# Performance work log

Hardware: AMD Instinct MI355X
Metric: run time of the kernel (lower is better)

The kernel has to match this reference:

```python
import jax, jax.numpy as jnp
import numpy as np

S, B, D = 2048, 2, 1024          # seq, batch, hidden
E, K = 64, 2                     # num_experts, top_k
I, SI = 512, 512                 # moe_intermediate, shared_expert_intermediate
CAP = 256                        # per-expert capacity; mean load = S*B*K/E = 128, 256 is >16 sigma -> no drops


def setup_inputs() -> dict:
    key = jax.random.key(0)
    ks = jax.random.split(key, 8)
    sc = lambda d: 1.0 / np.sqrt(d)
    return {
        "hidden_states": jax.random.normal(ks[0], (S, B, D), jnp.float32),
        "router_w": jax.random.normal(ks[1], (E, D), jnp.float32) * sc(D),          # FujiTopKRouter.weight
        "gate_up_proj": jax.random.normal(ks[2], (E, 2 * I, D), jnp.float32) * sc(D),
        "down_proj": jax.random.normal(ks[3], (E, D, I), jnp.float32) * sc(I),
        "sh_gate_w": jax.random.normal(ks[4], (SI, D), jnp.float32) * sc(D),
        "sh_up_w": jax.random.normal(ks[5], (SI, D), jnp.float32) * sc(D),
        "sh_down_w": jax.random.normal(ks[6], (D, SI), jnp.float32) * sc(SI),
        "sh_expert_gate_w": jax.random.normal(ks[7], (1, D), jnp.float32) * sc(D),
    }


def _moe(x, router_w, gate_up_proj, down_proj, sh_gate_w, sh_up_w, sh_down_w, sh_expert_gate_w):
    T = x.shape[0]
    # ---- shared expert (SwiGLU) + sigmoid gate ----
    shared = jnp.dot(jax.nn.silu(x @ sh_gate_w.T) * (x @ sh_up_w.T), sh_down_w.T)
    shared = jax.nn.sigmoid(x @ sh_expert_gate_w.T) * shared                      # [T, D]
    # ---- router: softmax (fp32) -> top-k -> normalize ----
    probs = jax.nn.softmax((x @ router_w.T).astype(jnp.float32), axis=-1)         # [T, E]
    top_w, top_i = jax.lax.top_k(probs, K)                                        # [T, K]
    top_w = top_w / (jnp.sum(top_w, axis=-1, keepdims=True) + 1e-9)
    top_w = top_w.astype(x.dtype)
    # ---- dispatch: permute (token, slot) pairs into fixed-capacity expert buffers ----
    e_f = top_i.reshape(-1)                                                       # [T*K] expert id per pair
    w_f = top_w.reshape(-1)                                                       # [T*K]
    tok = jnp.arange(T * K) // K                                                  # [T*K] source token
    oh = jax.nn.one_hot(e_f, E, dtype=jnp.int32)                                  # [T*K, E]
    pos = jnp.sum(jnp.cumsum(oh, axis=0) * oh, axis=-1) - 1                       # slot within expert
    buf = jnp.zeros((E, CAP, D), x.dtype).at[e_f, pos].set(x[tok])                # [E, C, D]
    # ---- per-expert SwiGLU as batched GEMMs ----
    h = jnp.einsum('ecd,eid->eci', buf, gate_up_proj)                             # [E, C, 2I]
    g, u = jnp.split(h, 2, axis=-1)
    y = jnp.einsum('eci,edi->ecd', jax.nn.silu(g) * u, down_proj)                 # [E, C, D]
    # ---- combine: gather back, weight, scatter-add to tokens ----
    routed = jnp.zeros_like(x).at[tok].add(y[e_f, pos] * w_f[:, None])            # [T, D]
    return shared + routed, probs


def reference(hidden_states, router_w, gate_up_proj, down_proj,
              sh_gate_w, sh_up_w, sh_down_w, sh_expert_gate_w):
    s, b, d = hidden_states.shape
    x = hidden_states.reshape(-1, d)
    out, router_logits = _moe(x, router_w, gate_up_proj, down_proj,
                              sh_gate_w, sh_up_w, sh_down_w, sh_expert_gate_w)
    return out.reshape(s, b, d), router_logits
```

## Files before the change

kernel.cpp:

```cpp
#include <hip/hip_runtime.h>
#include <hip/hip_bf16.h>
#include <stdint.h>

#define T_TOK 4096
#define DDIM  1024
#define NEXP  64
#define IDIM  512
#define SIDIM 512
#define CAP   256
#define KZ    8

typedef __attribute__((ext_vector_type(4))) float f32x4;
typedef __attribute__((ext_vector_type(8))) short bf16x8;

#define WAITV4 asm volatile("s_waitcnt vmcnt(4)" ::: "memory")
#define WAITV0 asm volatile("s_waitcnt vmcnt(0)" ::: "memory")
#define WAITL0 asm volatile("s_waitcnt lgkmcnt(0)" ::: "memory")
#define MEMBAR asm volatile("" ::: "memory")

__device__ __forceinline__ bf16x8 cvt8(f32x4 a, f32x4 b) {
    union { __hip_bfloat162 h[4]; bf16x8 v; } u;
    u.h[0] = __float22bfloat162_rn(make_float2(a[0], a[1]));
    u.h[1] = __float22bfloat162_rn(make_float2(a[2], a[3]));
    u.h[2] = __float22bfloat162_rn(make_float2(b[0], b[1]));
    u.h[3] = __float22bfloat162_rn(make_float2(b[2], b[3]));
    return u.v;
}
__device__ __forceinline__ short f2bs(float f) {
    union { __hip_bfloat16 h; short s; } u; u.h = __float2bfloat16(f); return u.s;
}

__device__ __forceinline__ void gload16(const void* g, void* l) {
    __builtin_amdgcn_global_load_lds((const __attribute__((address_space(1))) void*)g,
                                     (__attribute__((address_space(3))) void*)l, 16, 0, 0);
}

__device__ __forceinline__ bf16x8 frag32(const char* reg0, int row, int s) {
    const char* p = reg0 + row * 128;
    int sw = row & 7;
    f32x4 lo = *(const f32x4*)(p + (((2 * s) ^ sw) << 4));
    f32x4 hi = *(const f32x4*)(p + (((2 * s + 1) ^ sw) << 4));
    return cvt8(lo, hi);
}
__device__ __forceinline__ bf16x8 fragbf(const char* reg0, int row, int s) {
    return *(const bf16x8*)(reg0 + row * 64 + (((s) ^ (row & 3)) << 4));
}

__global__ __launch_bounds__(256) void logits_kernel(const float* __restrict__ X,
                                                     const float* __restrict__ RW,
                                                     float* __restrict__ lpart) {
    __shared__ float sX[64 * 33];
    __shared__ float sW[64 * 33];
    int m0 = blockIdx.x * 64;
    int kz = blockIdx.y;
    int kbase = kz * (DDIM / KZ);
    int tid = threadIdx.x;
    int tg = tid >> 4;
    int eg = tid & 15;
    float acc[4][4] = {};
    for (int k0 = 0; k0 < DDIM / KZ; k0 += 32) {
        __syncthreads();
#pragma unroll
        for (int i = 0; i < 8; ++i) {
            int idx = i * 256 + tid;
            int r = idx >> 5, c = idx & 31;
            sX[r * 33 + c] = X[(size_t)(m0 + r) * DDIM + kbase + k0 + c];
            sW[r * 33 + c] = RW[(size_t)r * DDIM + kbase + k0 + c];
        }
        __syncthreads();
#pragma unroll 4
        for (int k = 0; k < 32; ++k) {
            float xv[4], wv[4];
#pragma unroll
            for (int i = 0; i < 4; ++i) xv[i] = sX[(tg * 4 + i) * 33 + k];
#pragma unroll
            for (int j = 0; j < 4; ++j) wv[j] = sW[(eg * 4 + j) * 33 + k];
#pragma unroll
            for (int i = 0; i < 4; ++i)
#pragma unroll
                for (int j = 0; j < 4; ++j) acc[i][j] += xv[i] * wv[j];
        }
    }
    float* outp = lpart + (size_t)kz * T_TOK * NEXP;
#pragma unroll
    for (int i = 0; i < 4; ++i)
#pragma unroll
        for (int j = 0; j < 4; ++j)
            outp[(size_t)(m0 + tg * 4 + i) * NEXP + eg * 4 + j] = acc[i][j];
}

__global__ __launch_bounds__(256) void topk_kernel(const float* __restrict__ lpart,
                                                   const float* __restrict__ X,
                                                   const float* __restrict__ SEG,
                                                   float* __restrict__ probs_out,
                                                   int* __restrict__ counts,
                                                   int* __restrict__ tok_slot,
                                                   float* __restrict__ w_slot,
                                                   float* __restrict__ gate_sh) {
    int lane = threadIdx.x & 63;
    int wv   = threadIdx.x >> 6;
    int t    = blockIdx.x * 4 + wv;
    size_t li = (size_t)t * NEXP + lane;
    float l = 0.f;
#pragma unroll
    for (int z = 0; z < KZ; ++z) l += lpart[(size_t)z * T_TOK * NEXP + li];
    float mx = l;
    for (int s = 32; s; s >>= 1) mx = fmaxf(mx, __shfl_xor(mx, s));
    float e = __expf(l - mx);
    float sum = e;
    for (int s = 32; s; s >>= 1) sum += __shfl_xor(sum, s);
    float prob = e / sum;
    probs_out[li] = prob;
    float v = prob; int idx = lane;
    for (int s = 32; s; s >>= 1) {
        float ov = __shfl_xor(v, s); int oi = __shfl_xor(idx, s);
        if (ov > v || (ov == v && oi < idx)) { v = ov; idx = oi; }
    }
    float v1 = v; int i1 = idx;
    v = (lane == i1) ? -1e30f : prob; idx = lane;
    for (int s = 32; s; s >>= 1) {
        float ov = __shfl_xor(v, s); int oi = __shfl_xor(idx, s);
        if (ov > v || (ov == v && oi < idx)) { v = ov; idx = oi; }
    }
    float v2 = v; int i2 = idx;
    float denom = v1 + v2 + 1e-9f;
    if (lane == 0) {
        int s1 = atomicAdd(&counts[i1], 1);
        if (s1 < CAP) { tok_slot[i1 * CAP + s1] = t; w_slot[i1 * CAP + s1] = v1 / denom; }
        int s2 = atomicAdd(&counts[i2], 1);
        if (s2 < CAP) { tok_slot[i2 * CAP + s2] = t; w_slot[i2 * CAP + s2] = v2 / denom; }
    }
    float g = 0.f;
    const float* xr = X + (size_t)t * DDIM + lane * 16;
    const float* sr = SEG + lane * 16;
#pragma unroll
    for (int j = 0; j < 4; ++j) {
        f32x4 xv = *(const f32x4*)(xr + j * 4);
        f32x4 sv = *(const f32x4*)(sr + j * 4);
#pragma unroll
        for (int q = 0; q < 4; ++q) g += xv[q] * sv[q];
    }
    for (int s = 32; s; s >>= 1) g += __shfl_xor(g, s);
    if (lane == 0) gate_sh[t] = 1.f / (1.f + __expf(-g));
}

__global__ __launch_bounds__(256) void xgather(const float* __restrict__ X,
                                               const int* __restrict__ counts,
                                               const int* __restrict__ tok_slot,
                                               short* __restrict__ xg,
                                               short* __restrict__ xsh) {
    int b = blockIdx.x, tid = threadIdx.x;
    if (b < 512) {
        int r = b & 7, j = b >> 3;
        int e = (j & 7) * 8 + r;
        int s0 = (j >> 3) * 32;
        int M = counts[e]; if (M > CAP) M = CAP;
        for (int i = tid; i < 32 * 128; i += 256) {
            int sl = s0 + (i >> 7);
            int ch = i & 127;
            int src = (sl < M) ? tok_slot[e * CAP + sl] : 0;
            const float* p = X + (size_t)src * DDIM + ch * 8;
            f32x4 lo = *(const f32x4*)p, hi = *(const f32x4*)(p + 4);
            *(bf16x8*)(xg + ((size_t)e * CAP + sl) * DDIM + ch * 8) = cvt8(lo, hi);
        }
    } else {
        int r0 = (b - 512) * 32;
        for (int i = tid; i < 32 * 128; i += 256) {
            int row = r0 + (i >> 7), ch = i & 127;
            const float* p = X + (size_t)row * DDIM + ch * 8;
            f32x4 lo = *(const f32x4*)p, hi = *(const f32x4*)(p + 4);
            *(bf16x8*)(xsh + (size_t)row * DDIM + ch * 8) = cvt8(lo, hi);
        }
    }
}

__global__ __launch_bounds__(256, 2) void gateup_all(const short* __restrict__ xg,
                                                     const short* __restrict__ xsh,
                                                     const float* __restrict__ GUP,
                                                     const float* __restrict__ SG,
                                                     const float* __restrict__ SU,
                                                     const int* __restrict__ counts,
                                                     short* __restrict__ act,
                                                     short* __restrict__ act_sh) {
    __shared__ char sA[2 * 8192];
    __shared__ char sB[3 * 16384];
    const int NS = DDIM / 32;
    int f = blockIdx.x;
    bool expert = f < 1024;
    int e = 0, m0, n0, M;
    const float *Wg, *Wu;
    const short* Abase;
    short* act_out;
    size_t out_base, arow0;
    if (expert) {
        int r = f & 7, q = (f >> 3) & 7, n = (f >> 6) & 7, y = f >> 9;
        e = q * 8 + r;
        n0 = n * 64; m0 = y * 128;
        M = counts[e]; if (M > CAP) M = CAP;
        if (m0 >= M) return;
        const float* base = GUP + (size_t)e * (2 * IDIM) * DDIM;
        Wg = base; Wu = base + (size_t)IDIM * DDIM;
        Abase = xg; arow0 = (size_t)e * CAP + m0;
        act_out = act; out_base = (size_t)e * CAP * IDIM;
    } else {
        int g = f - 1024;
        int mp = g & 31, n = g >> 5;
        n0 = n * 64; m0 = mp * 128;
        M = T_TOK; Wg = SG; Wu = SU;
        Abase = xsh; arow0 = (size_t)m0;
        act_out = act_sh; out_base = 0;
    }
    int tid = threadIdx.x, lane = tid & 63, wv = tid >> 6;
    int wm = wv >> 1, wn = wv & 1;

    const short* apA[2];
#pragma unroll
    for (int t = 0; t < 2; ++t) {
        int row = (t * 4 + wv) * 16 + (lane >> 2);
        int slot = (lane & 3) ^ ((lane >> 2) & 3);
        apA[t] = Abase + (arow0 + row) * DDIM + slot * 8;
    }
    const float* bpB[4];
#pragma unroll
    for (int t = 0; t < 2; ++t) {
        int row = (t * 4 + wv) * 8 + (lane >> 3);
        int slot = (lane & 7) ^ ((lane >> 3) & 7);
        bpB[t]     = Wg + (size_t)(n0 + row) * DDIM + slot * 4;
        bpB[2 + t] = Wu + (size_t)(n0 + row) * DDIM + slot * 4;
    }

    auto issueA = [&](int s) {
        char* base = sA + (s & 1) * 8192;
#pragma unroll
        for (int t = 0; t < 2; ++t)
            gload16(apA[t] + s * 32, base + (t * 4 + wv) * 1024);
    };
    auto issueB = [&](int s) {
        char* base = sB + (s % 3) * 16384;
#pragma unroll
        for (int t = 0; t < 2; ++t) {
            gload16(bpB[t] + s * 32,     base + (t * 4 + wv) * 1024);
            gload16(bpB[2 + t] + s * 32, base + 8192 + (t * 4 + wv) * 1024);
        }
    };

    int fm = lane & 15, sk = lane >> 4;
    f32x4 accg[4][2] = {}, accu[4][2] = {};
    auto compute = [&](int s) {
        const char* bbA = sA + (s & 1) * 8192;
        const char* bbB = sB + (s % 3) * 16384;
        bf16x8 bg[2], bu[2];
#pragma unroll
        for (int nt = 0; nt < 2; ++nt) {
            int row = wn * 32 + nt * 16 + fm;
            bg[nt] = frag32(bbB, row, sk);
            bu[nt] = frag32(bbB + 8192, row, sk);
        }
#pragma unroll
        for (int mt = 0; mt < 4; ++mt) {
            int row = wm * 64 + mt * 16 + fm;
            bf16x8 a = fragbf(bbA, row, sk);
#pragma unroll
            for (int nt = 0; nt < 2; ++nt) {
                accg[mt][nt] = __builtin_amdgcn_mfma_f32_16x16x32_bf16(a, bg[nt], accg[mt][nt], 0, 0, 0);
                accu[mt][nt] = __builtin_amdgcn_mfma_f32_16x16x32_bf16(a, bu[nt], accu[mt][nt], 0, 0, 0);
            }
        }
    };

    issueA(0); issueB(0); issueB(1);
#pragma unroll 1
    for (int s = 0; s < NS; ++s) {
        if (s < NS - 1) { WAITV4; } else { WAITV0; }
        WAITL0;
        __builtin_amdgcn_s_barrier();
        MEMBAR;
        if (s + 1 < NS) issueA(s + 1);
        if (s + 2 < NS) issueB(s + 2);
        compute(s);
    }

    int frow = (lane >> 4) * 4, fcol = lane & 15;
#pragma unroll
    for (int mt = 0; mt < 4; ++mt)
#pragma unroll
        for (int r = 0; r < 4; ++r) {
            int row = m0 + wm * 64 + mt * 16 + frow + r;
            if (row < M) {
#pragma unroll
                for (int nt = 0; nt < 2; ++nt) {
                    float g = accg[mt][nt][r];
                    float u = accu[mt][nt][r];
                    float a = (g / (1.f + __expf(-g))) * u;
                    act_out[out_base + (size_t)row * IDIM + (n0 + wn * 32 + nt * 16 + fcol)] = f2bs(a);
                }
            }
        }
}

__global__ __launch_bounds__(256, 2) void down_all(const short* __restrict__ act,
                                                   const short* __restrict__ act_sh,
                                                   const float* __restrict__ DW,
                                                   const float* __restrict__ SD,
                                                   const int* __restrict__ counts,
                                                   const int* __restrict__ tok_slot,
                                                   const float* __restrict__ w_slot,
                                                   const float* __restrict__ gate_sh,
                                                   float* __restrict__ out) {
    __shared__ char sA[2 * 8192];
    __shared__ char sB[3 * 16384];
    const int KD = IDIM;
    const int NS = KD / 32;
    int f = blockIdx.x;
    bool expert = f < 1024;
    int e = 0, m0, n0, M;
    const short* A;
    const float* W;
    if (expert) {
        int r = f & 7, q = (f >> 3) & 7, n = (f >> 6) & 7, y = f >> 9;
        e = q * 8 + r;
        n0 = n * 128; m0 = y * 128;
        M = counts[e]; if (M > CAP) M = CAP;
        if (m0 >= M) return;
        A = act + (size_t)e * CAP * IDIM;
        W = DW + (size_t)e * DDIM * IDIM;
    } else {
        int g = f - 1024;
        int mp = g & 31, n = g >> 5;
        n0 = n * 128; m0 = mp * 128;
        M = T_TOK; A = act_sh; W = SD;
    }
    int tid = threadIdx.x, lane = tid & 63, wv = tid >> 6;
    int wm = wv >> 1, wn = wv & 1;

    const short* apA[2];
#pragma unroll
    for (int t = 0; t < 2; ++t) {
        int row = (t * 4 + wv) * 16 + (lane >> 2);
        int slot = (lane & 3) ^ ((lane >> 2) & 3);
        apA[t] = A + (size_t)(m0 + row) * KD + slot * 8;
    }
    const float* bpB[4];
#pragma unroll
    for (int t = 0; t < 4; ++t) {
        int row = (t * 4 + wv) * 8 + (lane >> 3);
        int slot = (lane & 7) ^ ((lane >> 3) & 7);
        bpB[t] = W + (size_t)(n0 + row) * KD + slot * 4;
    }

    auto issueA = [&](int s) {
        char* base = sA + (s & 1) * 8192;
#pragma unroll
        for (int t = 0; t < 2; ++t)
            gload16(apA[t] + s * 32, base + (t * 4 + wv) * 1024);
    };
    auto issueB = [&](int s) {
        char* base = sB + (s % 3) * 16384;
#pragma unroll
        for (int t = 0; t < 4; ++t)
            gload16(bpB[t] + s * 32, base + (t * 4 + wv) * 1024);
    };

    int fm = lane & 15, sk = lane >> 4;
    f32x4 acc[4][4] = {};
    auto compute = [&](int s) {
        const char* bbA = sA + (s & 1) * 8192;
        const char* bbB = sB + (s % 3) * 16384;
        bf16x8 b[4];
#pragma unroll
        for (int nt = 0; nt < 4; ++nt) {
            int row = wn * 64 + nt * 16 + fm;
            b[nt] = frag32(bbB, row, sk);
        }
#pragma unroll
        for (int mt = 0; mt < 4; ++mt) {
            int row = wm * 64 + mt * 16 + fm;
            bf16x8 a = fragbf(bbA, row, sk);
#pragma unroll
            for (int nt = 0; nt < 4; ++nt)
                acc[mt][nt] = __builtin_amdgcn_mfma_f32_16x16x32_bf16(a, b[nt], acc[mt][nt], 0, 0, 0);
        }
    };

    issueA(0); issueB(0); issueB(1);
#pragma unroll 1
    for (int s = 0; s < NS; ++s) {
        if (s < NS - 1) { WAITV4; } else { WAITV0; }
        WAITL0;
        __builtin_amdgcn_s_barrier();
        MEMBAR;
        if (s + 1 < NS) issueA(s + 1);
        if (s + 2 < NS) issueB(s + 2);
        compute(s);
    }

    int frow = (lane >> 4) * 4, fcol = lane & 15;
#pragma unroll
    for (int mt = 0; mt < 4; ++mt)
#pragma unroll
        for (int r = 0; r < 4; ++r) {
            int row = m0 + wm * 64 + mt * 16 + frow + r;
            if (row >= M) continue;
            float scale; int trow;
            if (expert) { scale = w_slot[e * CAP + row]; trow = tok_slot[e * CAP + row]; }
            else        { scale = gate_sh[row];          trow = row; }
#pragma unroll
            for (int nt = 0; nt < 4; ++nt) {
                int col = n0 + wn * 64 + nt * 16 + fcol;
                atomicAdd(&out[(size_t)trow * DDIM + col], acc[mt][nt][r] * scale);
            }
        }
}

extern "C" void kernel_launch(void* const* d_in, const int* in_sizes, int n_in,
                              void* d_out, int out_size, void* d_ws, size_t ws_size,
                              hipStream_t stream) {
    const float* X   = (const float*)d_in[0];
    const float* RW  = (const float*)d_in[1];
    const float* GUP = (const float*)d_in[2];
    const float* DW  = (const float*)d_in[3];
    const float* SG  = (const float*)d_in[4];
    const float* SU  = (const float*)d_in[5];
    const float* SD  = (const float*)d_in[6];
    const float* SEG = (const float*)d_in[7];
    float* out = (float*)d_out;

    char* ws = (char*)d_ws;
    size_t off = 0;
    float* lpart    = (float*)(ws + off); off += (size_t)KZ * T_TOK * NEXP * 4;
    int*   counts   = (int*)  (ws + off); off += 1024;
    int*   tok_slot = (int*)  (ws + off); off += (size_t)NEXP * CAP * 4;
    float* w_slot   = (float*)(ws + off); off += (size_t)NEXP * CAP * 4;
    float* gate_sh  = (float*)(ws + off); off += (size_t)T_TOK * 4;
    short* act      = (short*)(ws + off); off += (size_t)NEXP * CAP * IDIM * 2;
    short* act_sh   = (short*)(ws + off); off += (size_t)T_TOK * SIDIM * 2;
    short* xg       = (short*)(ws + off); off += (size_t)NEXP * CAP * DDIM * 2;
    short* xsh      = (short*)(ws + off); off += (size_t)T_TOK * DDIM * 2;
    (void)ws_size; (void)in_sizes; (void)n_in; (void)out_size;

    hipMemsetAsync(counts, 0, NEXP * sizeof(int), stream);
    hipMemsetAsync(out, 0, (size_t)T_TOK * DDIM * sizeof(float), stream);
    logits_kernel<<<dim3(T_TOK / 64, KZ), 256, 0, stream>>>(X, RW, lpart);
    topk_kernel<<<T_TOK / 4, 256, 0, stream>>>(lpart, X, SEG,
                                               out + (size_t)T_TOK * DDIM,
                                               counts, tok_slot, w_slot, gate_sh);
    xgather<<<640, 256, 0, stream>>>(X, counts, tok_slot, xg, xsh);
    gateup_all<<<1280, 256, 0, stream>>>(xg, xsh, GUP, SG, SU, counts, act, act_sh);
    down_all<<<1280, 256, 0, stream>>>(act, act_sh, DW, SD, counts, tok_slot,
                                       w_slot, gate_sh, out);
}
```

Baseline: 694.5 us.

## Pre-convert expert weights to bf16 and simplify GEMM pipelines to double-buffered smem

Adds a conversion kernel that turns all expert and shared-expert weights from fp32 to bf16 in the workspace on every call. The GEMM kernels then load bf16 weight tiles directly, with no per-fragment fp32 to bf16 conversion, and the shared-memory footprint drops from 64KB to 32KB so occupancy can go to 4 blocks per CU. The 3-stage custom-waitcnt pipeline is replaced by a plain double buffer with __syncthreads. The risk is the extra full weight read and write every call (about 200MB of fp32 read) plus less latency hiding from the simpler pipeline.

```diff
diff --git a/kernel.cpp b/kernel.cpp
--- a/kernel.cpp
+++ b/kernel.cpp
@@ -13,11 +13,6 @@
 typedef __attribute__((ext_vector_type(4))) float f32x4;
 typedef __attribute__((ext_vector_type(8))) short bf16x8;
 
-#define WAITV4 asm volatile("s_waitcnt vmcnt(4)" ::: "memory")
-#define WAITV0 asm volatile("s_waitcnt vmcnt(0)" ::: "memory")
-#define WAITL0 asm volatile("s_waitcnt lgkmcnt(0)" ::: "memory")
-#define MEMBAR asm volatile("" ::: "memory")
-
 __device__ __forceinline__ bf16x8 cvt8(f32x4 a, f32x4 b) {
     union { __hip_bfloat162 h[4]; bf16x8 v; } u;
     u.h[0] = __float22bfloat162_rn(make_float2(a[0], a[1]));
@@ -35,15 +30,19 @@
                                      (__attribute__((address_space(3))) void*)l, 16, 0, 0);
 }
 
-__device__ __forceinline__ bf16x8 frag32(const char* reg0, int row, int s) {
-    const char* p = reg0 + row * 128;
-    int sw = row & 7;
-    f32x4 lo = *(const f32x4*)(p + (((2 * s) ^ sw) << 4));
-    f32x4 hi = *(const f32x4*)(p + (((2 * s + 1) ^ sw) << 4));
-    return cvt8(lo, hi);
-}
-__device__ __forceinline__ bf16x8 fragbf(const char* reg0, int row, int s) {
-    return *(const bf16x8*)(reg0 + row * 64 + (((s) ^ (row & 3)) << 4));
+__device__ __forceinline__ bf16x8 fragbf(const char* base, int row, int sk) {
+    return *(const bf16x8*)(base + row * 64 + ((sk ^ ((row >> 1) & 3)) << 4));
+}
+
+__global__ __launch_bounds__(256) void cvtw(const float* __restrict__ src,
+                                            short* __restrict__ dst, int n8) {
+    int i = blockIdx.x * blockDim.x + threadIdx.x;
+    int stride = gridDim.x * blockDim.x;
+    for (; i < n8; i += stride) {
+        f32x4 lo = *(const f32x4*)(src + (size_t)i * 8);
+        f32x4 hi = *(const f32x4*)(src + (size_t)i * 8 + 4);
+        *(bf16x8*)(dst + (size_t)i * 8) = cvt8(lo, hi);
+    }
 }
 
 __global__ __launch_bounds__(256) void logits_kernel(const float* __restrict__ X,
@@ -174,22 +173,20 @@
     }
 }
 
-__global__ __launch_bounds__(256, 2) void gateup_all(const short* __restrict__ xg,
+__global__ __launch_bounds__(256, 4) void gateup_all(const short* __restrict__ xg,
                                                      const short* __restrict__ xsh,
-                                                     const float* __restrict__ GUP,
-                                                     const float* __restrict__ SG,
-                                                     const float* __restrict__ SU,
+                                                     const short* __restrict__ gupb,
+                                                     const short* __restrict__ sgb,
+                                                     const short* __restrict__ subw,
                                                      const int* __restrict__ counts,
                                                      short* __restrict__ act,
                                                      short* __restrict__ act_sh) {
-    __shared__ char sA[2 * 8192];
-    __shared__ char sB[3 * 16384];
+    __shared__ char smem[2 * 16384];
     const int NS = DDIM / 32;
     int f = blockIdx.x;
     bool expert = f < 1024;
     int e = 0, m0, n0, M;
-    const float *Wg, *Wu;
-    const short* Abase;
+    const short *Wgb, *Wub, *Abase;
     short* act_out;
     size_t out_base, arow0;
     if (expert) {
@@ -198,68 +195,53 @@
         n0 = n * 64; m0 = y * 128;
         M = counts[e]; if (M > CAP) M = CAP;
         if (m0 >= M) return;
-        const float* base = GUP + (size_t)e * (2 * IDIM) * DDIM;
-        Wg = base; Wu = base + (size_t)IDIM * DDIM;
+        Wgb = gupb + (size_t)e * (2 * IDIM) * DDIM;
+        Wub = Wgb + (size_t)IDIM * DDIM;
         Abase = xg; arow0 = (size_t)e * CAP + m0;
         act_out = act; out_base = (size_t)e * CAP * IDIM;
     } else {
         int g = f - 1024;
         int mp = g & 31, n = g >> 5;
         n0 = n * 64; m0 = mp * 128;
-        M = T_TOK; Wg = SG; Wu = SU;
+        M = T_TOK; Wgb = sgb; Wub = subw;
         Abase = xsh; arow0 = (size_t)m0;
         act_out = act_sh; out_base = 0;
     }
     int tid = threadIdx.x, lane = tid & 63, wv = tid >> 6;
     int wm = wv >> 1, wn = wv & 1;
 
-    const short* apA[2];
-#pragma unroll
-    for (int t = 0; t < 2; ++t) {
-        int row = (t * 4 + wv) * 16 + (lane >> 2);
-        int slot = (lane & 3) ^ ((lane >> 2) & 3);
-        apA[t] = Abase + (arow0 + row) * DDIM + slot * 8;
-    }
-    const float* bpB[4];
-#pragma unroll
-    for (int t = 0; t < 2; ++t) {
-        int row = (t * 4 + wv) * 8 + (lane >> 3);
-        int slot = (lane & 7) ^ ((lane >> 3) & 7);
-        bpB[t]     = Wg + (size_t)(n0 + row) * DDIM + slot * 4;
-        bpB[2 + t] = Wu + (size_t)(n0 + row) * DDIM + slot * 4;
-    }
-
-    auto issueA = [&](int s) {
-        char* base = sA + (s & 1) * 8192;
-#pragma unroll
-        for (int t = 0; t < 2; ++t)
-            gload16(apA[t] + s * 32, base + (t * 4 + wv) * 1024);
-    };
-    auto issueB = [&](int s) {
-        char* base = sB + (s % 3) * 16384;
-#pragma unroll
-        for (int t = 0; t < 2; ++t) {
-            gload16(bpB[t] + s * 32,     base + (t * 4 + wv) * 1024);
-            gload16(bpB[2 + t] + s * 32, base + 8192 + (t * 4 + wv) * 1024);
-        }
+    int gsl = (lane & 3) ^ ((lane >> 3) & 3);
+    int crow = wv * 16 + (lane >> 2);
+    const short* gpA0 = Abase + (arow0 + crow) * DDIM + gsl * 8;
+    const short* gpA1 = Abase + (arow0 + crow + 64) * DDIM + gsl * 8;
+    const short* gpBg = Wgb + (size_t)(n0 + crow) * DDIM + gsl * 8;
+    const short* gpBu = Wub + (size_t)(n0 + crow) * DDIM + gsl * 8;
+    int oA0 = wv * 1024, oA1 = (wv + 4) * 1024;
+    int oBg = 8192 + wv * 1024, oBu = 12288 + wv * 1024;
+
+    auto issue = [&](int buf, int s) {
+        char* base = smem + buf * 16384;
+        int k = s * 32;
+        gload16(gpA0 + k, base + oA0);
+        gload16(gpA1 + k, base + oA1);
+        gload16(gpBg + k, base + oBg);
+        gload16(gpBu + k, base + oBu);
     };
 
     int fm = lane & 15, sk = lane >> 4;
     f32x4 accg[4][2] = {}, accu[4][2] = {};
-    auto compute = [&](int s) {
-        const char* bbA = sA + (s & 1) * 8192;
-        const char* bbB = sB + (s % 3) * 16384;
+    auto compute = [&](int buf) {
+        const char* base = smem + buf * 16384;
         bf16x8 bg[2], bu[2];
 #pragma unroll
         for (int nt = 0; nt < 2; ++nt) {
             int row = wn * 32 + nt * 16 + fm;
-            bg[nt] = frag32(bbB, row, sk);
-            bu[nt] = frag32(bbB + 8192, row, sk);
+            bg[nt] = fragbf(base + 8192, row, sk);
+            bu[nt] = fragbf(base + 12288, row, sk);
         }
 #pragma unroll
         for (int mt = 0; mt < 4; ++mt) {
-            int row = wm * 64 + mt * 16 + fm;
-            bf16x8 a = fragbf(bbA, row, sk);
+            bf16x8 a = fragbf(base, wm * 64 + mt * 16 + fm, sk);
 #pragma unroll
             for (int nt = 0; nt < 2; ++nt) {
                 accg[mt][nt] = __builtin_amdgcn_mfma_f32_16x16x32_bf16(a, bg[nt], accg[mt][nt], 0, 0, 0);
@@ -268,16 +250,15 @@
         }
     };
 
-    issueA(0); issueB(0); issueB(1);
+    issue(0, 0);
 #pragma unroll 1
-    for (int s = 0; s < NS; ++s) {
-        if (s < NS - 1) { WAITV4; } else { WAITV0; }
-        WAITL0;
-        __builtin_amdgcn_s_barrier();
-        MEMBAR;
-        if (s + 1 < NS) issueA(s + 1);
-        if (s + 2 < NS) issueB(s + 2);
-        compute(s);
+    for (int s = 0; s < NS; s += 2) {
+        __syncthreads();
+        if (s + 1 < NS) issue(1, s + 1);
+        compute(0);
+        __syncthreads();
+        if (s + 2 < NS) issue(0, s + 2);
+        compute(1);
     }
 
     int frow = (lane >> 4) * 4, fcol = lane & 15;
@@ -298,24 +279,22 @@
         }
 }
 
-__global__ __launch_bounds__(256, 2) void down_all(const short* __restrict__ act,
+__global__ __launch_bounds__(256, 4) void down_all(const short* __restrict__ act,
                                                    const short* __restrict__ act_sh,
-                                                   const float* __restrict__ DW,
-                                                   const float* __restrict__ SD,
+                                                   const short* __restrict__ dwb,
+                                                   const short* __restrict__ sdb,
                                                    const int* __restrict__ counts,
                                                    const int* __restrict__ tok_slot,
                                                    const float* __restrict__ w_slot,
                                                    const float* __restrict__ gate_sh,
                                                    float* __restrict__ out) {
-    __shared__ char sA[2 * 8192];
-    __shared__ char sB[3 * 16384];
+    __shared__ char smem[2 * 16384];
     const int KD = IDIM;
     const int NS = KD / 32;
     int f = blockIdx.x;
     bool expert = f < 1024;
     int e = 0, m0, n0, M;
-    const short* A;
-    const float* W;
+    const short *A, *W;
     if (expert) {
         int r = f & 7, q = (f >> 3) & 7, n = (f >> 6) & 7, y = f >> 9;
         e = q * 8 + r;
@@ -323,75 +302,60 @@
         M = counts[e]; if (M > CAP) M = CAP;
         if (m0 >= M) return;
         A = act + (size_t)e * CAP * IDIM;
-        W = DW + (size_t)e * DDIM * IDIM;
+        W = dwb + (size_t)e * DDIM * IDIM;
     } else {
         int g = f - 1024;
         int mp = g & 31, n = g >> 5;
         n0 = n * 128; m0 = mp * 128;
-        M = T_TOK; A = act_sh; W = SD;
+        M = T_TOK; A = act_sh; W = sdb;
     }
     int tid = threadIdx.x, lane = tid & 63, wv = tid >> 6;
     int wm = wv >> 1, wn = wv & 1;
 
-    const short* apA[2];
-#pragma unroll
-    for (int t = 0; t < 2; ++t) {
-        int row = (t * 4 + wv) * 16 + (lane >> 2);
-        int slot = (lane & 3) ^ ((lane >> 2) & 3);
-        apA[t] = A + (size_t)(m0 + row) * KD + slot * 8;
-    }
-    const float* bpB[4];
-#pragma unroll
-    for (int t = 0; t < 4; ++t) {
-        int row = (t * 4 + wv) * 8 + (lane >> 3);
-        int slot = (lane & 7) ^ ((lane >> 3) & 7);
-        bpB[t] = W + (size_t)(n0 + row) * KD + slot * 4;
-    }
-
-    auto issueA = [&](int s) {
-        char* base = sA + (s & 1) * 8192;
-#pragma unroll
-        for (int t = 0; t < 2; ++t)
-            gload16(apA[t] + s * 32, base + (t * 4 + wv) * 1024);
-    };
-    auto issueB = [&](int s) {
-        char* base = sB + (s % 3) * 16384;
-#pragma unroll
-        for (int t = 0; t < 4; ++t)
-            gload16(bpB[t] + s * 32, base + (t * 4 + wv) * 1024);
+    int gsl = (lane & 3) ^ ((lane >> 3) & 3);
+    int crow = wv * 16 + (lane >> 2);
+    const short* gpA0 = A + (size_t)(m0 + crow) * KD + gsl * 8;
+    const short* gpA1 = A + (size_t)(m0 + crow + 64) * KD + gsl * 8;
+    const short* gpB0 = W + (size_t)(n0 + crow) * KD + gsl * 8;
+    const short* gpB1 = W + (size_t)(n0 + crow + 64) * KD + gsl * 8;
+    int oA0 = wv * 1024, oA1 = (wv + 4) * 1024;
+    int oB0 = 8192 + wv * 1024, oB1 = 8192 + (wv + 4) * 1024;
+
+    auto issue = [&](int buf, int s) {
+        char* base = smem + buf * 16384;
+        int k = s * 32;
+        gload16(gpA0 + k, base + oA0);
+        gload16(gpA1 + k, base + oA1);
+        gload16(gpB0 + k, base + oB0);
+        gload16(gpB1 + k, base + oB1);
     };
 
     int fm = lane & 15, sk = lane >> 4;
     f32x4 acc[4][4] = {};
-    auto compute = [&](int s) {
-        const char* bbA = sA + (s & 1) * 8192;
-        const char* bbB = sB + (s % 3) * 16384;
+    auto compute = [&](int buf) {
+        const char* base = smem + buf * 16384;
         bf16x8 b[4];
 #pragma unroll
-        for (int nt = 0; nt < 4; ++nt) {
-            int row = wn * 64 + nt * 16 + fm;
-            b[nt] = frag32(bbB, row, sk);
-        }
+        for (int nt = 0; nt < 4; ++nt)
+            b[nt] = fragbf(base + 8192, wn * 64 + nt * 16 + fm, sk);
 #pragma unroll
         for (int mt = 0; mt < 4; ++mt) {
-            int row = wm * 64 + mt * 16 + fm;
-            bf16x8 a = fragbf(bbA, row, sk);
+            bf16x8 a = fragbf(base, wm * 64 + mt * 16 + fm, sk);
 #pragma unroll
             for (int nt = 0; nt < 4; ++nt)
                 acc[mt][nt] = __builtin_amdgcn_mfma_f32_16x16x32_bf16(a, b[nt], acc[mt][nt], 0, 0, 0);
         }
     };
 
-    issueA(0); issueB(0); issueB(1);
+    issue(0, 0);
 #pragma unroll 1
-    for (int s = 0; s < NS; ++s) {
-        if (s < NS - 1) { WAITV4; } else { WAITV0; }
-        WAITL0;
-        __builtin_amdgcn_s_barrier();
-        MEMBAR;
-        if (s + 1 < NS) issueA(s + 1);
-        if (s + 2 < NS) issueB(s + 2);
-        compute(s);
+    for (int s = 0; s < NS; s += 2) {
+        __syncthreads();
+        if (s + 1 < NS) issue(1, s + 1);
+        compute(0);
+        __syncthreads();
+        if (s + 2 < NS) issue(0, s + 2);
+        compute(1);
     }
 
     int frow = (lane >> 4) * 4, fcol = lane & 15;
@@ -436,16 +400,28 @@
     short* act_sh   = (short*)(ws + off); off += (size_t)T_TOK * SIDIM * 2;
     short* xg       = (short*)(ws + off); off += (size_t)NEXP * CAP * DDIM * 2;
     short* xsh      = (short*)(ws + off); off += (size_t)T_TOK * DDIM * 2;
+    short* gupb     = (short*)(ws + off); off += (size_t)NEXP * 2 * IDIM * DDIM * 2;
+    short* dwb      = (short*)(ws + off); off += (size_t)NEXP * DDIM * IDIM * 2;
+    short* sgb      = (short*)(ws + off); off += (size_t)SIDIM * DDIM * 2;
+    short* subw     = (short*)(ws + off); off += (size_t)SIDIM * DDIM * 2;
+    short* sdb      = (short*)(ws + off); off += (size_t)DDIM * SIDIM * 2;
     (void)ws_size; (void)in_sizes; (void)n_in; (void)out_size;
 
     hipMemsetAsync(counts, 0, NEXP * sizeof(int), stream);
     hipMemsetAsync(out, 0, (size_t)T_TOK * DDIM * sizeof(float), stream);
+
+    cvtw<<<2048, 256, 0, stream>>>(GUP, gupb, NEXP * 2 * IDIM * DDIM / 8);
+    cvtw<<<2048, 256, 0, stream>>>(DW, dwb, NEXP * DDIM * IDIM / 8);
+    cvtw<<<256, 256, 0, stream>>>(SG, sgb, SIDIM * DDIM / 8);
+    cvtw<<<256, 256, 0, stream>>>(SU, subw, SIDIM * DDIM / 8);
+    cvtw<<<256, 256, 0, stream>>>(SD, sdb, DDIM * SIDIM / 8);
+
     logits_kernel<<<dim3(T_TOK / 64, KZ), 256, 0, stream>>>(X, RW, lpart);
     topk_kernel<<<T_TOK / 4, 256, 0, stream>>>(lpart, X, SEG,
                                                out + (size_t)T_TOK * DDIM,
                                                counts, tok_slot, w_slot, gate_sh);
     xgather<<<640, 256, 0, stream>>>(X, counts, tok_slot, xg, xsh);
-    gateup_all<<<1280, 256, 0, stream>>>(xg, xsh, GUP, SG, SU, counts, act, act_sh);
-    down_all<<<1280, 256, 0, stream>>>(act, act_sh, DW, SD, counts, tok_slot,
+    gateup_all<<<1280, 256, 0, stream>>>(xg, xsh, gupb, sgb, subw, counts, act, act_sh);
+    down_all<<<1280, 256, 0, stream>>>(act, act_sh, dwb, sdb, counts, tok_slot,
                                        w_slot, gate_sh, out);
 }
```

Result: no change. 697.5 us (+0.4%).

## Replace LDS-staged GEMM pipelines with direct register loads of MFMA fragments

Applied to the files above, without the earlier changes.

Both grouped GEMM kernels (gate/up and down) drop the shared-memory staging through global_load_lds, triple buffering and barriers. Each lane now loads its own MFMA fragments straight from global memory into registers, with a two-stage register double buffer. This removes LDS traffic and per-step barriers. The cost is that waves sharing a tile no longer share loads, so global/L2 traffic rises and each row is read in short strided chunks. Register pressure also goes up.

```diff
diff --git a/kernel.cpp b/kernel.cpp
--- a/kernel.cpp
+++ b/kernel.cpp
@@ -13,11 +13,6 @@
 typedef __attribute__((ext_vector_type(4))) float f32x4;
 typedef __attribute__((ext_vector_type(8))) short bf16x8;
 
-#define WAITV4 asm volatile("s_waitcnt vmcnt(4)" ::: "memory")
-#define WAITV0 asm volatile("s_waitcnt vmcnt(0)" ::: "memory")
-#define WAITL0 asm volatile("s_waitcnt lgkmcnt(0)" ::: "memory")
-#define MEMBAR asm volatile("" ::: "memory")
-
 __device__ __forceinline__ bf16x8 cvt8(f32x4 a, f32x4 b) {
     union { __hip_bfloat162 h[4]; bf16x8 v; } u;
     u.h[0] = __float22bfloat162_rn(make_float2(a[0], a[1]));
@@ -28,22 +23,6 @@
 }
 __device__ __forceinline__ short f2bs(float f) {
     union { __hip_bfloat16 h; short s; } u; u.h = __float2bfloat16(f); return u.s;
-}
-
-__device__ __forceinline__ void gload16(const void* g, void* l) {
-    __builtin_amdgcn_global_load_lds((const __attribute__((address_space(1))) void*)g,
-                                     (__attribute__((address_space(3))) void*)l, 16, 0, 0);
-}
-
-__device__ __forceinline__ bf16x8 frag32(const char* reg0, int row, int s) {
-    const char* p = reg0 + row * 128;
-    int sw = row & 7;
-    f32x4 lo = *(const f32x4*)(p + (((2 * s) ^ sw) << 4));
-    f32x4 hi = *(const f32x4*)(p + (((2 * s + 1) ^ sw) << 4));
-    return cvt8(lo, hi);
-}
-__device__ __forceinline__ bf16x8 fragbf(const char* reg0, int row, int s) {
-    return *(const bf16x8*)(reg0 + row * 64 + (((s) ^ (row & 3)) << 4));
 }
 
 __global__ __launch_bounds__(256) void logits_kernel(const float* __restrict__ X,
@@ -182,9 +161,6 @@
                                                      const int* __restrict__ counts,
                                                      short* __restrict__ act,
                                                      short* __restrict__ act_sh) {
-    __shared__ char sA[2 * 8192];
-    __shared__ char sB[3 * 16384];
-    const int NS = DDIM / 32;
     int f = blockIdx.x;
     bool expert = f < 1024;
     int e = 0, m0, n0, M;
@@ -193,91 +169,77 @@
     short* act_out;
     size_t out_base, arow0;
     if (expert) {
-        int r = f & 7, q = (f >> 3) & 7, n = (f >> 6) & 7, y = f >> 9;
+        int r = f & 7, q = (f >> 3) & 7;
         e = q * 8 + r;
-        n0 = n * 64; m0 = y * 128;
+        n0 = ((f >> 6) & 7) * 64;
+        m0 = ((f >> 9) & 1) * 128;
         M = counts[e]; if (M > CAP) M = CAP;
         if (m0 >= M) return;
-        const float* base = GUP + (size_t)e * (2 * IDIM) * DDIM;
-        Wg = base; Wu = base + (size_t)IDIM * DDIM;
+        Wg = GUP + (size_t)e * (2 * IDIM) * DDIM;
+        Wu = Wg + (size_t)IDIM * DDIM;
         Abase = xg; arow0 = (size_t)e * CAP + m0;
         act_out = act; out_base = (size_t)e * CAP * IDIM;
     } else {
         int g = f - 1024;
-        int mp = g & 31, n = g >> 5;
-        n0 = n * 64; m0 = mp * 128;
+        m0 = (g & 31) * 128; n0 = ((g >> 5) & 7) * 64;
         M = T_TOK; Wg = SG; Wu = SU;
         Abase = xsh; arow0 = (size_t)m0;
         act_out = act_sh; out_base = 0;
     }
     int tid = threadIdx.x, lane = tid & 63, wv = tid >> 6;
     int wm = wv >> 1, wn = wv & 1;
-
-    const short* apA[2];
-#pragma unroll
-    for (int t = 0; t < 2; ++t) {
-        int row = (t * 4 + wv) * 16 + (lane >> 2);
-        int slot = (lane & 3) ^ ((lane >> 2) & 3);
-        apA[t] = Abase + (arow0 + row) * DDIM + slot * 8;
-    }
-    const float* bpB[4];
-#pragma unroll
-    for (int t = 0; t < 2; ++t) {
-        int row = (t * 4 + wv) * 8 + (lane >> 3);
-        int slot = (lane & 7) ^ ((lane >> 3) & 7);
-        bpB[t]     = Wg + (size_t)(n0 + row) * DDIM + slot * 4;
-        bpB[2 + t] = Wu + (size_t)(n0 + row) * DDIM + slot * 4;
-    }
-
-    auto issueA = [&](int s) {
-        char* base = sA + (s & 1) * 8192;
-#pragma unroll
-        for (int t = 0; t < 2; ++t)
-            gload16(apA[t] + s * 32, base + (t * 4 + wv) * 1024);
+    int fm = lane & 15, sk = lane >> 4;
+
+    const short* apA[4];
+#pragma unroll
+    for (int mt = 0; mt < 4; ++mt)
+        apA[mt] = Abase + (arow0 + wm * 64 + mt * 16 + fm) * DDIM + sk * 8;
+    const float *bpg[2], *bpu[2];
+#pragma unroll
+    for (int nt = 0; nt < 2; ++nt) {
+        int row = n0 + wn * 32 + nt * 16 + fm;
+        bpg[nt] = Wg + (size_t)row * DDIM + sk * 8;
+        bpu[nt] = Wu + (size_t)row * DDIM + sk * 8;
+    }
+
+    struct R { bf16x8 a[4]; f32x4 g[4]; f32x4 u[4]; };
+    R r0, r1;
+    auto load = [&](R& r, int k) {
+#pragma unroll
+        for (int mt = 0; mt < 4; ++mt) r.a[mt] = *(const bf16x8*)(apA[mt] + k);
+#pragma unroll
+        for (int nt = 0; nt < 2; ++nt) {
+            r.g[2 * nt]     = *(const f32x4*)(bpg[nt] + k);
+            r.g[2 * nt + 1] = *(const f32x4*)(bpg[nt] + k + 4);
+            r.u[2 * nt]     = *(const f32x4*)(bpu[nt] + k);
+            r.u[2 * nt + 1] = *(const f32x4*)(bpu[nt] + k + 4);
+        }
     };
-    auto issueB = [&](int s) {
-        char* base = sB + (s % 3) * 16384;
-#pragma unroll
-        for (int t = 0; t < 2; ++t) {
-            gload16(bpB[t] + s * 32,     base + (t * 4 + wv) * 1024);
-            gload16(bpB[2 + t] + s * 32, base + 8192 + (t * 4 + wv) * 1024);
+    f32x4 accg[4][2] = {}, accu[4][2] = {};
+    auto compute = [&](const R& r) {
+        bf16x8 bg[2], bu[2];
+#pragma unroll
+        for (int nt = 0; nt < 2; ++nt) {
+            bg[nt] = cvt8(r.g[2 * nt], r.g[2 * nt + 1]);
+            bu[nt] = cvt8(r.u[2 * nt], r.u[2 * nt + 1]);
+        }
+#pragma unroll
+        for (int mt = 0; mt < 4; ++mt) {
+#pragma unroll
+            for (int nt = 0; nt < 2; ++nt) {
+                accg[mt][nt] = __builtin_amdgcn_mfma_f32_16x16x32_bf16(r.a[mt], bg[nt], accg[mt][nt], 0, 0, 0);
+                accu[mt][nt] = __builtin_amdgcn_mfma_f32_16x16x32_bf16(r.a[mt], bu[nt], accu[mt][nt], 0, 0, 0);
+            }
         }
     };
 
-    int fm = lane & 15, sk = lane >> 4;
-    f32x4 accg[4][2] = {}, accu[4][2] = {};
-    auto compute = [&](int s) {
-        const char* bbA = sA + (s & 1) * 8192;
-        const char* bbB = sB + (s % 3) * 16384;
-        bf16x8 bg[2], bu[2];
-#pragma unroll
-        for (int nt = 0; nt < 2; ++nt) {
-            int row = wn * 32 + nt * 16 + fm;
-            bg[nt] = frag32(bbB, row, sk);
-            bu[nt] = frag32(bbB + 8192, row, sk);
-        }
-#pragma unroll
-        for (int mt = 0; mt < 4; ++mt) {
-            int row = wm * 64 + mt * 16 + fm;
-            bf16x8 a = fragbf(bbA, row, sk);
-#pragma unroll
-            for (int nt = 0; nt < 2; ++nt) {
-                accg[mt][nt] = __builtin_amdgcn_mfma_f32_16x16x32_bf16(a, bg[nt], accg[mt][nt], 0, 0, 0);
-                accu[mt][nt] = __builtin_amdgcn_mfma_f32_16x16x32_bf16(a, bu[nt], accu[mt][nt], 0, 0, 0);
-            }
-        }
-    };
-
-    issueA(0); issueB(0); issueB(1);
+    load(r0, 0);
 #pragma unroll 1
-    for (int s = 0; s < NS; ++s) {
-        if (s < NS - 1) { WAITV4; } else { WAITV0; }
-        WAITL0;
-        __builtin_amdgcn_s_barrier();
-        MEMBAR;
-        if (s + 1 < NS) issueA(s + 1);
-        if (s + 2 < NS) issueB(s + 2);
-        compute(s);
+    for (int k = 0; k < DDIM; k += 64) {
+        load(r1, k + 32);
+        compute(r0);
+        load(r0, (k + 64 < DDIM) ? (k + 64) : 0);
+        compute(r1);
     }
 
     int frow = (lane >> 4) * 4, fcol = lane & 15;
@@ -307,91 +269,69 @@
                                                    const float* __restrict__ w_slot,
                                                    const float* __restrict__ gate_sh,
                                                    float* __restrict__ out) {
-    __shared__ char sA[2 * 8192];
-    __shared__ char sB[3 * 16384];
     const int KD = IDIM;
-    const int NS = KD / 32;
     int f = blockIdx.x;
     bool expert = f < 1024;
     int e = 0, m0, n0, M;
     const short* A;
     const float* W;
     if (expert) {
-        int r = f & 7, q = (f >> 3) & 7, n = (f >> 6) & 7, y = f >> 9;
+        int r = f & 7, q = (f >> 3) & 7;
         e = q * 8 + r;
-        n0 = n * 128; m0 = y * 128;
+        n0 = ((f >> 6) & 7) * 128;
+        m0 = ((f >> 9) & 1) * 128;
         M = counts[e]; if (M > CAP) M = CAP;
         if (m0 >= M) return;
         A = act + (size_t)e * CAP * IDIM;
         W = DW + (size_t)e * DDIM * IDIM;
     } else {
         int g = f - 1024;
-        int mp = g & 31, n = g >> 5;
-        n0 = n * 128; m0 = mp * 128;
+        m0 = (g & 31) * 128; n0 = ((g >> 5) & 7) * 128;
         M = T_TOK; A = act_sh; W = SD;
     }
     int tid = threadIdx.x, lane = tid & 63, wv = tid >> 6;
     int wm = wv >> 1, wn = wv & 1;
-
-    const short* apA[2];
-#pragma unroll
-    for (int t = 0; t < 2; ++t) {
-        int row = (t * 4 + wv) * 16 + (lane >> 2);
-        int slot = (lane & 3) ^ ((lane >> 2) & 3);
-        apA[t] = A + (size_t)(m0 + row) * KD + slot * 8;
-    }
-    const float* bpB[4];
-#pragma unroll
-    for (int t = 0; t < 4; ++t) {
-        int row = (t * 4 + wv) * 8 + (lane >> 3);
-        int slot = (lane & 7) ^ ((lane >> 3) & 7);
-        bpB[t] = W + (size_t)(n0 + row) * KD + slot * 4;
-    }
-
-    auto issueA = [&](int s) {
-        char* base = sA + (s & 1) * 8192;
-#pragma unroll
-        for (int t = 0; t < 2; ++t)
-            gload16(apA[t] + s * 32, base + (t * 4 + wv) * 1024);
+    int fm = lane & 15, sk = lane >> 4;
+
+    const short* apA[4];
+#pragma unroll
+    for (int mt = 0; mt < 4; ++mt)
+        apA[mt] = A + (size_t)(m0 + wm * 64 + mt * 16 + fm) * KD + sk * 8;
+    const float* bp[4];
+#pragma unroll
+    for (int nt = 0; nt < 4; ++nt)
+        bp[nt] = W + (size_t)(n0 + wn * 64 + nt * 16 + fm) * KD + sk * 8;
+
+    struct R { bf16x8 a[4]; f32x4 b[8]; };
+    R r0, r1;
+    auto load = [&](R& r, int k) {
+#pragma unroll
+        for (int mt = 0; mt < 4; ++mt) r.a[mt] = *(const bf16x8*)(apA[mt] + k);
+#pragma unroll
+        for (int nt = 0; nt < 4; ++nt) {
+            r.b[2 * nt]     = *(const f32x4*)(bp[nt] + k);
+            r.b[2 * nt + 1] = *(const f32x4*)(bp[nt] + k + 4);
+        }
     };
-    auto issueB = [&](int s) {
-        char* base = sB + (s % 3) * 16384;
-#pragma unroll
-        for (int t = 0; t < 4; ++t)
-            gload16(bpB[t] + s * 32, base + (t * 4 + wv) * 1024);
+    f32x4 acc[4][4] = {};
+    auto compute = [&](const R& r) {
+        bf16x8 b[4];
+#pragma unroll
+        for (int nt = 0; nt < 4; ++nt) b[nt] = cvt8(r.b[2 * nt], r.b[2 * nt + 1]);
+#pragma unroll
+        for (int mt = 0; mt < 4; ++mt)
+#pragma unroll
+            for (int nt = 0; nt < 4; ++nt)
+                acc[mt][nt] = __builtin_amdgcn_mfma_f32_16x16x32_bf16(r.a[mt], b[nt], acc[mt][nt], 0, 0, 0);
     };
 
-    int fm = lane & 15, sk = lane >> 4;
-    f32x4 acc[4][4] = {};
-    auto compute = [&](int s) {
-        const char* bbA = sA + (s & 1) * 8192;
-        const char* bbB = sB + (s % 3) * 16384;
-        bf16x8 b[4];
-#pragma unroll
-        for (int nt = 0; nt < 4; ++nt) {
-            int row = wn * 64 + nt * 16 + fm;
-            b[nt] = frag32(bbB, row, sk);
-        }
-#pragma unroll
-        for (int mt = 0; mt < 4; ++mt) {
-            int row = wm * 64 + mt * 16 + fm;
-            bf16x8 a = fragbf(bbA, row, sk);
-#pragma unroll
-            for (int nt = 0; nt < 4; ++nt)
-                acc[mt][nt] = __builtin_amdgcn_mfma_f32_16x16x32_bf16(a, b[nt], acc[mt][nt], 0, 0, 0);
-        }
-    };
-
-    issueA(0); issueB(0); issueB(1);
+    load(r0, 0);
 #pragma unroll 1
-    for (int s = 0; s < NS; ++s) {
-        if (s < NS - 1) { WAITV4; } else { WAITV0; }
-        WAITL0;
-        __builtin_amdgcn_s_barrier();
-        MEMBAR;
-        if (s + 1 < NS) issueA(s + 1);
-        if (s + 2 < NS) issueB(s + 2);
-        compute(s);
+    for (int k = 0; k < KD; k += 64) {
+        load(r1, k + 32);
+        compute(r0);
+        load(r0, (k + 64 < KD) ? (k + 64) : 0);
+        compute(r1);
     }
 
     int frow = (lane >> 4) * 4, fcol = lane & 15;
@@ -440,6 +380,7 @@
 
     hipMemsetAsync(counts, 0, NEXP * sizeof(int), stream);
     hipMemsetAsync(out, 0, (size_t)T_TOK * DDIM * sizeof(float), stream);
+
     logits_kernel<<<dim3(T_TOK / 64, KZ), 256, 0, stream>>>(X, RW, lpart);
     topk_kernel<<<T_TOK / 4, 256, 0, stream>>>(lpart, X, SEG,
                                                out + (size_t)T_TOK * DDIM,
```

Measured after the change: 918.0 us. 1.32x slower.
